# Kernel tuning notes

Hardware: AMD Instinct MI355X
Metric: run time of the kernel (lower is better)

The kernel has to match this reference:

```python
import jax, jax.numpy as jnp
import numpy as np

G = 512          # graphs per batch
NPG = 90         # nodes per graph (AAL-90 atlas)
N = G * NPG      # 46080 total nodes
DEG = 20
E = N * DEG      # 921600 edges
F_IN = 90
H = 64           # hidden_channels (args.hc)
K = 70           # sort-pool k


def setup_inputs() -> dict:
    key = jax.random.key(0)
    ks = jax.random.split(key, 14)
    x = jax.random.normal(ks[0], (N, F_IN), dtype=jnp.float32)
    # edges kept within each graph (realistic PyG batching)
    gid = jax.random.randint(ks[1], (E,), 0, G)
    src = gid * NPG + jax.random.randint(ks[2], (E,), 0, NPG)
    dst = gid * NPG + jax.random.randint(ks[3], (E,), 0, NPG)
    edge_index = jnp.stack([src, dst]).astype(jnp.int64)
    batch = (jnp.arange(N) // NPG).astype(jnp.int64)
    s_in = 1.0 / np.sqrt(F_IN)
    s_h = 1.0 / np.sqrt(H)
    s_p = 1.0 / np.sqrt(H * K)
    # SAGEConv: out = mean_aggr(x_j) @ W_l + x_i @ W_r + b
    W1l = jax.random.uniform(ks[4], (F_IN, H), jnp.float32, -s_in, s_in)
    W1r = jax.random.uniform(ks[5], (F_IN, H), jnp.float32, -s_in, s_in)
    b1 = jnp.zeros((H,), jnp.float32)
    W2l = jax.random.uniform(ks[6], (H, H), jnp.float32, -s_h, s_h)
    W2r = jax.random.uniform(ks[7], (H, H), jnp.float32, -s_h, s_h)
    b2 = jnp.zeros((H,), jnp.float32)
    Wl1 = jax.random.uniform(ks[8], (H * K, H), jnp.float32, -s_p, s_p)
    bl1 = jax.random.uniform(ks[9], (H,), jnp.float32, -s_p, s_p)
    Wl2 = jax.random.uniform(ks[10], (H, 1), jnp.float32, -s_h, s_h)
    bl2 = jax.random.uniform(ks[11], (1,), jnp.float32, -s_h, s_h)
    return {"x": x, "edge_index": edge_index, "batch": batch,
            "W1l": W1l, "W1r": W1r, "b1": b1,
            "W2l": W2l, "W2r": W2r, "b2": b2,
            "Wl1": Wl1, "bl1": bl1, "Wl2": Wl2, "bl2": bl2}


def sage_conv(x, src, dst, Wl, Wr, b):
    # gather source features, scatter-mean to destinations
    msg = x[src]                                              # [E, F]
    s = jax.ops.segment_sum(msg, dst, num_segments=N)         # [N, F]
    cnt = jax.ops.segment_sum(jnp.ones((src.shape[0], 1), x.dtype),
                              dst, num_segments=N)            # [N, 1]
    mean = s / jnp.maximum(cnt, 1.0)
    return mean @ Wl + x @ Wr + b


def global_sort_pool(x, k):
    # nodes per graph are contiguous and fixed (NPG >= k, no padding needed)
    xr = x.reshape(G, NPG, H)
    order = jnp.argsort(-xr[:, :, -1], axis=1)[:, :k]          # sort by last channel, desc
    top = jnp.take_along_axis(xr, order[:, :, None], axis=1)   # [G, k, H]
    return top.reshape(G, k * H)


def reference(x, edge_index, batch, W1l, W1r, b1, W2l, W2r, b2, Wl1, bl1, Wl2, bl2):
    src, dst = edge_index[0], edge_index[1]
    h = sage_conv(x, src, dst, W1l, W1r, b1)       # conv1
    x_train = h
    h = jax.nn.relu(h)
    h = sage_conv(h, src, dst, W2l, W2r, b2)       # conv2
    p = global_sort_pool(h, K)                     # [G, K*H]
    # dropout is identity at eval time
    p = p @ Wl1 + bl1
    p = p @ Wl2 + bl2
    out = jnp.squeeze(jax.nn.sigmoid(p))           # [G]
    return out, x_train
```

## Files before the change

### kernel.cpp

```cpp
#include <hip/hip_runtime.h>

typedef unsigned short u16;
typedef unsigned int u32;
typedef unsigned char u8;
typedef unsigned long long u64;

#define GG   512
#define NPG  90
#define NTOT (GG*NPG)
#define NED  921600
#define FIN  90
#define HC   64
#define KP   70
#define AW   23
#define AWG  (NPG*AW)

#define SAD  91
#define SP   68
#define SR   67

#define WF_W1L 0
#define WF_W1R 5760
#define WF_W2L 11520
#define WF_W2R 15616
#define WF_B1  19712
#define WF_B2  19776
#define WF_FOLD 19840
#define WF_ZC  24320
#define WF_FLAG 24321

__device__ __forceinline__ float bf2f(u16 u) {
    union { u32 i; float f; } v; v.i = ((u32)u) << 16; return v.f;
}
__device__ __forceinline__ float bflo(u32 u) {
    union { u32 i; float f; } v; v.i = u << 16; return v.f;
}
__device__ __forceinline__ float bfhi(u32 u) {
    union { u32 i; float f; } v; v.i = u & 0xFFFF0000u; return v.f;
}
__device__ __forceinline__ u16 f2bf(float f) {
    union { float f; u32 i; } v; v.f = f;
    u32 r = (v.i + 0x7FFFu + ((v.i >> 16) & 1u)) >> 16;
    return (u16)r;
}
__device__ __forceinline__ float ldadp(const void* p, long long i, int isf32) {
    return isf32 ? ((const float*)p)[i] : bf2f(((const u16*)p)[i]);
}

__global__ __launch_bounds__(256) void k_pre(
    const u32* __restrict__ xw, const int* __restrict__ ei,
    const void* W1l, const void* W1r, const void* b1,
    const void* W2l, const void* W2r, const void* b2,
    const void* Wl1, const void* bl1, const void* Wl2, const void* bl2,
    u32* __restrict__ A32, float* __restrict__ wf)
{
    __shared__ int sf;
    const int t = threadIdx.x;
    const int b = blockIdx.x;

    if (b < 900) {
        int lane = t & 63;
        u32 v = (lane < 16) ? (u32)ei[lane] : 0u;
        u64 bb = __ballot((lane & 1) && (v != 0));
        bool wide = (bb == 0ull);
        int e0 = b * 1024 + t * 4;
        int s[4], d[4];
        if (wide) {
            uint4 s01 = *(const uint4*)(ei + 2 * e0);
            uint4 s23 = *(const uint4*)(ei + 2 * e0 + 4);
            uint4 d01 = *(const uint4*)(ei + 2 * (NED + e0));
            uint4 d23 = *(const uint4*)(ei + 2 * (NED + e0) + 4);
            s[0] = (int)s01.x; s[1] = (int)s01.z; s[2] = (int)s23.x; s[3] = (int)s23.z;
            d[0] = (int)d01.x; d[1] = (int)d01.z; d[2] = (int)d23.x; d[3] = (int)d23.z;
        } else {
            uint4 ss = *(const uint4*)(ei + e0);
            uint4 dd = *(const uint4*)(ei + NED + e0);
            s[0] = (int)ss.x; s[1] = (int)ss.y; s[2] = (int)ss.z; s[3] = (int)ss.w;
            d[0] = (int)dd.x; d[1] = (int)dd.y; d[2] = (int)dd.z; d[3] = (int)dd.w;
        }
        #pragma unroll
        for (int k = 0; k < 4; ++k) {
            int dk = d[k];
            if ((unsigned)dk >= NTOT) continue;
            int g = (unsigned)dk / NPG;
            int dl = dk - g * NPG;
            int ls = s[k] - g * NPG;
            if ((unsigned)ls >= NPG) continue;
            atomicAdd(&A32[(size_t)g * AWG + dl * AW + (ls >> 2)],
                      1u << (8 * (ls & 3)));
        }
        return;
    }

    if (t < 64) {
        u32 e = (xw[t] >> 7) & 0xFF;
        u64 bb = __ballot(e >= 136);
        if (t == 0) sf = (bb != 0ull) ? 1 : 0;
    }
    __syncthreads();
    const int f32 = sf;

    if (b < 978) {
        int i = (b - 900) * 256 + t;
        if      (i < 5760)  wf[i] = ldadp(W1l, i, f32);
        else if (i < 11520) wf[i] = ldadp(W1r, i - 5760, f32);
        else if (i < 15616) wf[i] = ldadp(W2l, i - 11520, f32);
        else if (i < 19712) wf[i] = ldadp(W2r, i - 15616, f32);
        else if (i < 19776) wf[i] = ldadp(b1, i - 19712, f32);
        else if (i < 19840) wf[i] = ldadp(b2, i - 19776, f32);
        if (b == 900 && t == 0) wf[WF_FLAG] = f32 ? 1.0f : 0.0f;
    } else {
        int m = (b - 978) * 256 + t;
        if (m < 4480) {
            float s = 0.f;
            for (int j = 0; j < HC; ++j)
                s += ldadp(Wl1, (long long)m * HC + j, f32) * ldadp(Wl2, j, f32);
            wf[WF_FOLD + m] = s;
        } else if (m == 4480) {
            float s = ldadp(bl2, 0, f32);
            for (int j = 0; j < HC; ++j)
                s += ldadp(bl1, j, f32) * ldadp(Wl2, j, f32);
            wf[WF_ZC] = s;
        }
    }
}

__global__ __launch_bounds__(512, 4) void k_fused(
    const void* __restrict__ x, const u32* __restrict__ A32,
    const float* __restrict__ wf, void* __restrict__ dout)
{
    __shared__ __align__(16) char smem[58144];
    float* As    = (float*)smem;
    float* R1    = (float*)(smem + 32768);
    float* s_key = (float*)(smem + 57248);
    float* s_red = (float*)(smem + 57968);
    u16*   s_ord = (u16*)(smem + 58000);

    const int g = blockIdx.x;
    const int t = threadIdx.x;
    const bool isf32 = (wf[WF_FLAG] > 0.5f);

    const int l = t & 63;
    const int w = __builtin_amdgcn_readfirstlane(t >> 6);
    const int jb = w * 8;
    const int row0 = l;
    const bool has2 = (l < NPG - 64);
    const int row1 = has2 ? l + 64 : l;

    u32 abuf[5];
    {
        const u32* Ag = A32 + (size_t)g * AWG;
        #pragma unroll
        for (int j = 0; j < 5; ++j) {
            int p = t + j * 512;
            abuf[j] = (p < AWG) ? Ag[p] : 0u;
        }
    }

    if (isf32) {
        const float* xg = (const float*)x + (size_t)g * 8100;
        for (int p = t; p < 8100; p += 512) {
            int r = p / NPG, c = p - r * NPG;
            As[r * SAD + c] = xg[p];
        }
    } else {
        const u32* xg = (const u32*)((const u16*)x + (size_t)g * 8100);
        for (int p = t; p < 4050; p += 512) {
            int r = p / 45, c = (p - r * 45) * 2;
            u32 v = xg[p];
            As[r * SAD + c]     = bflo(v);
            As[r * SAD + c + 1] = bfhi(v);
        }
    }
    __syncthreads();

    float accP[2][8], accQ[2][8];
    {
        const float* bb = wf + WF_B1 + jb;
        #pragma unroll
        for (int j = 0; j < 8; ++j) {
            float bv = bb[j];
            accP[0][j] = 0.f; accP[1][j] = 0.f;
            accQ[0][j] = bv;  accQ[1][j] = bv;
        }
    }
    {
        const float* WL = wf + WF_W1L + jb;
        const float* WR = wf + WF_W1R + jb;
        #pragma unroll 3
        for (int k = 0; k < FIN; ++k) {
            float wl[8], wr[8];
            #pragma unroll
            for (int j = 0; j < 8; ++j) { wl[j] = WL[k * HC + j]; wr[j] = WR[k * HC + j]; }
            float x0 = As[row0 * SAD + k];
            float x1 = As[row1 * SAD + k];
            #pragma unroll
            for (int j = 0; j < 8; ++j) {
                accP[0][j] += x0 * wl[j]; accQ[0][j] += x0 * wr[j];
                accP[1][j] += x1 * wl[j]; accQ[1][j] += x1 * wr[j];
            }
        }
    }
    __syncthreads();

    *(float4*)(R1 + row0 * SP + jb)     = make_float4(accP[0][0], accP[0][1], accP[0][2], accP[0][3]);
    *(float4*)(R1 + row0 * SP + jb + 4) = make_float4(accP[0][4], accP[0][5], accP[0][6], accP[0][7]);
    if (has2) {
        *(float4*)(R1 + row1 * SP + jb)     = make_float4(accP[1][0], accP[1][1], accP[1][2], accP[1][3]);
        *(float4*)(R1 + row1 * SP + jb + 4) = make_float4(accP[1][4], accP[1][5], accP[1][6], accP[1][7]);
    }
    #pragma unroll
    for (int j = 0; j < 5; ++j) {
        int p = t + j * 512;
        if (p < AWG) {
            int r = p / AW, wc = p - r * AW;
            int c = wc * 4;
            u32 v = abuf[j];
            float* dst = As + r * SAD + c;
            dst[0] = (float)(v & 255u);
            dst[1] = (float)((v >> 8) & 255u);
            dst[2] = (float)((v >> 16) & 255u);
            if (c + 3 < SAD) dst[3] = (float)(v >> 24);
        }
    }
    __syncthreads();

    float r1v[2][8];
    float rc0, rc1;
    {
        float acc[2][8];
        float asum0 = 0.f, asum1 = 0.f;
        #pragma unroll
        for (int i = 0; i < 2; ++i)
            #pragma unroll
            for (int j = 0; j < 8; ++j) acc[i][j] = 0.f;
        for (int k = 0; k < NPG; ++k) {
            float4 p0 = *(const float4*)(R1 + k * SP + jb);
            float4 p1 = *(const float4*)(R1 + k * SP + jb + 4);
            float pv[8] = {p0.x,p0.y,p0.z,p0.w,p1.x,p1.y,p1.z,p1.w};
            float a0 = As[row0 * SAD + k];
            float a1 = As[row1 * SAD + k];
            asum0 += a0; asum1 += a1;
            #pragma unroll
            for (int j = 0; j < 8; ++j) {
                acc[0][j] += a0 * pv[j];
                acc[1][j] += a1 * pv[j];
            }
        }
        rc0 = 1.0f / fmaxf(asum0, 1.0f);
        rc1 = 1.0f / fmaxf(asum1, 1.0f);
        #pragma unroll
        for (int i = 0; i < 2; ++i) {
            if (i == 0 || has2) {
                int n = i ? row1 : row0;
                float rc = i ? rc1 : rc0;
                float h[8];
                #pragma unroll
                for (int j = 0; j < 8; ++j) h[j] = fmaf(rc, acc[i][j], accQ[i][j]);
                size_t base = 512 + (size_t)(g * NPG + n) * HC + jb;
                if (isf32) {
                    *(float4*)((float*)dout + base)     = make_float4(h[0],h[1],h[2],h[3]);
                    *(float4*)((float*)dout + base + 4) = make_float4(h[4],h[5],h[6],h[7]);
                } else {
                    uint4 pk;
                    pk.x = (u32)f2bf(h[0]) | ((u32)f2bf(h[1]) << 16);
                    pk.y = (u32)f2bf(h[2]) | ((u32)f2bf(h[3]) << 16);
                    pk.z = (u32)f2bf(h[4]) | ((u32)f2bf(h[5]) << 16);
                    pk.w = (u32)f2bf(h[6]) | ((u32)f2bf(h[7]) << 16);
                    *(uint4*)((u16*)dout + base) = pk;
                }
                #pragma unroll
                for (int j = 0; j < 8; ++j) r1v[i][j] = fmaxf(h[j], 0.f);
            }
        }
    }
    __syncthreads();
    #pragma unroll
    for (int j = 0; j < 8; ++j) R1[row0 * SR + jb + j] = r1v[0][j];
    if (has2) {
        #pragma unroll
        for (int j = 0; j < 8; ++j) R1[row1 * SR + jb + j] = r1v[1][j];
    }
    __syncthreads();

    {
        const float* bb = wf + WF_B2 + jb;
        #pragma unroll
        for (int j = 0; j < 8; ++j) {
            float bv = bb[j];
            accP[0][j] = 0.f; accP[1][j] = 0.f;
            accQ[0][j] = bv;  accQ[1][j] = bv;
        }
    }
    {
        const float* WL = wf + WF_W2L + jb;
        const float* WR = wf + WF_W2R + jb;
        #pragma unroll 4
        for (int k = 0; k < HC; ++k) {
            float wl[8], wr[8];
            #pragma unroll
            for (int j = 0; j < 8; ++j) { wl[j] = WL[k * HC + j]; wr[j] = WR[k * HC + j]; }
            float v0 = R1[row0 * SR + k];
            float v1 = R1[row1 * SR + k];
            #pragma unroll
            for (int j = 0; j < 8; ++j) {
                accP[0][j] += v0 * wl[j]; accQ[0][j] += v0 * wr[j];
                accP[1][j] += v1 * wl[j]; accQ[1][j] += v1 * wr[j];
            }
        }
    }
    __syncthreads();
    *(float4*)(R1 + row0 * SP + jb)     = make_float4(accP[0][0], accP[0][1], accP[0][2], accP[0][3]);
    *(float4*)(R1 + row0 * SP + jb + 4) = make_float4(accP[0][4], accP[0][5], accP[0][6], accP[0][7]);
    if (has2) {
        *(float4*)(R1 + row1 * SP + jb)     = make_float4(accP[1][0], accP[1][1], accP[1][2], accP[1][3]);
        *(float4*)(R1 + row1 * SP + jb + 4) = make_float4(accP[1][4], accP[1][5], accP[1][6], accP[1][7]);
    }
    __syncthreads();

    float h2v[2][8];
    {
        float acc[2][8];
        #pragma unroll
        for (int i = 0; i < 2; ++i)
            #pragma unroll
            for (int j = 0; j < 8; ++j) acc[i][j] = 0.f;
        for (int k = 0; k < NPG; ++k) {
            float4 p0 = *(const float4*)(R1 + k * SP + jb);
            float4 p1 = *(const float4*)(R1 + k * SP + jb + 4);
            float pv[8] = {p0.x,p0.y,p0.z,p0.w,p1.x,p1.y,p1.z,p1.w};
            float a0 = As[row0 * SAD + k];
            float a1 = As[row1 * SAD + k];
            #pragma unroll
            for (int j = 0; j < 8; ++j) {
                acc[0][j] += a0 * pv[j];
                acc[1][j] += a1 * pv[j];
            }
        }
        #pragma unroll
        for (int i = 0; i < 2; ++i) {
            if (i == 0 || has2) {
                int n = i ? row1 : row0;
                float rc = i ? rc1 : rc0;
                #pragma unroll
                for (int j = 0; j < 8; ++j)
                    h2v[i][j] = fmaf(rc, acc[i][j], accQ[i][j]);
                if (w == 7) s_key[n] = h2v[i][7];
            }
        }
    }
    __syncthreads();
    #pragma unroll
    for (int j = 0; j < 8; ++j) R1[row0 * SR + jb + j] = h2v[0][j];
    if (has2) {
        #pragma unroll
        for (int j = 0; j < 8; ++j) R1[row1 * SR + jb + j] = h2v[1][j];
    }
    if (t < NPG) {
        float my = s_key[t];
        int r = 0;
        for (int m2 = 0; m2 < NPG; ++m2) {
            float km = s_key[m2];
            r += (km > my) || (km == my && m2 < t);
        }
        if (r < KP) s_ord[r] = (u16)t;
    }
    __syncthreads();

    float zp = 0.f;
    for (int p = t; p < KP * HC; p += 512) {
        int i = p >> 6, c = p & 63;
        int nn = s_ord[i];
        zp += R1[nn * SR + c] * wf[WF_FOLD + p];
    }
    #pragma unroll
    for (int off = 32; off > 0; off >>= 1) zp += __shfl_down(zp, off);
    if ((t & 63) == 0) s_red[t >> 6] = zp;
    __syncthreads();
    if (t == 0) {
        float z = wf[WF_ZC];
        #pragma unroll
        for (int i = 0; i < 8; ++i) z += s_red[i];
        float sg = 1.0f / (1.0f + expf(-z));
        if (isf32) ((float*)dout)[g] = sg;
        else       ((u16*)dout)[g]   = f2bf(sg);
    }
}

extern "C" void kernel_launch(void* const* d_in, const int* in_sizes, int n_in,
                              void* d_out, int out_size, void* d_ws, size_t ws_size,
                              hipStream_t stream) {
    const void* x   = d_in[0];
    const int*  ei  = (const int*)d_in[1];
    const void* W1l = d_in[3];
    const void* W1r = d_in[4];
    const void* b1  = d_in[5];
    const void* W2l = d_in[6];
    const void* W2r = d_in[7];
    const void* b2  = d_in[8];
    const void* Wl1 = d_in[9];
    const void* bl1 = d_in[10];
    const void* Wl2 = d_in[11];
    const void* bl2 = d_in[12];

    char* ws    = (char*)d_ws;
    u32*  A32   = (u32*)ws;
    float* wf   = (float*)(ws + 4239360);

    hipMemsetAsync(A32, 0, 4239360, stream);
    k_pre<<<996, 256, 0, stream>>>((const u32*)x, ei, W1l, W1r, b1, W2l, W2r, b2,
                                   Wl1, bl1, Wl2, bl2, A32, wf);
    k_fused<<<GG, 512, 0, stream>>>(x, A32, wf, d_out);
}
```

Before: 183.1 us.

## Fuse memset, preprocessing and main kernel into one cooperative launch

Replaces the memset, the k_pre kernel and k_fused with a single cooperative kernel that uses grid.sync barriers. Each block zeroes its own adjacency slice, converts a share of the weights and loads its x tile, then after a grid sync scatters edges with atomics and, after a second sync, runs the shared compute pipeline. The aim is to remove launch gaps and the separate memset pass and to keep x resident in LDS. In exchange it relies on all 512 blocks being co-resident and adds two grid-wide barriers; the old three-launch path remains as a fallback if the cooperative launch fails.

```diff
diff --git a/kernel.cpp b/kernel.cpp
--- a/kernel.cpp
+++ b/kernel.cpp
@@ -1,4 +1,7 @@
 #include <hip/hip_runtime.h>
+#include <hip/hip_cooperative_groups.h>
+
+namespace cg = cooperative_groups;
 
 typedef unsigned short u16;
 typedef unsigned int u32;
@@ -45,6 +48,365 @@
 }
 __device__ __forceinline__ float ldadp(const void* p, long long i, int isf32) {
     return isf32 ? ((const float*)p)[i] : bf2f(((const u16*)p)[i]);
+}
+
+struct CParams {
+    const float* wf;
+    void* dout;
+    int g, t;
+    bool isf32;
+};
+
+__device__ __forceinline__ void pipeline_C(
+    float* As, float* R1, float* s_key, float* s_red, u16* s_ord,
+    const u32* abuf , const CParams& P)
+{
+    const int g = P.g, t = P.t;
+    const bool isf32 = P.isf32;
+    const float* wf = P.wf;
+    void* dout = P.dout;
+
+    const int l = t & 63;
+    const int w = __builtin_amdgcn_readfirstlane(t >> 6);
+    const int jb = w * 8;
+    const int row0 = l;
+    const bool has2 = (l < NPG - 64);
+    const int row1 = has2 ? l + 64 : l;
+
+    float accP[2][8], accQ[2][8];
+    {
+        const float* bb = wf + WF_B1 + jb;
+        #pragma unroll
+        for (int j = 0; j < 8; ++j) {
+            float bv = bb[j];
+            accP[0][j] = 0.f; accP[1][j] = 0.f;
+            accQ[0][j] = bv;  accQ[1][j] = bv;
+        }
+    }
+    {
+        const float* WL = wf + WF_W1L + jb;
+        const float* WR = wf + WF_W1R + jb;
+        #pragma unroll 3
+        for (int k = 0; k < FIN; ++k) {
+            float wl[8], wr[8];
+            #pragma unroll
+            for (int j = 0; j < 8; ++j) { wl[j] = WL[k * HC + j]; wr[j] = WR[k * HC + j]; }
+            float x0 = As[row0 * SAD + k];
+            float x1 = As[row1 * SAD + k];
+            #pragma unroll
+            for (int j = 0; j < 8; ++j) {
+                accP[0][j] += x0 * wl[j]; accQ[0][j] += x0 * wr[j];
+                accP[1][j] += x1 * wl[j]; accQ[1][j] += x1 * wr[j];
+            }
+        }
+    }
+    __syncthreads();
+
+    *(float4*)(R1 + row0 * SP + jb)     = make_float4(accP[0][0], accP[0][1], accP[0][2], accP[0][3]);
+    *(float4*)(R1 + row0 * SP + jb + 4) = make_float4(accP[0][4], accP[0][5], accP[0][6], accP[0][7]);
+    if (has2) {
+        *(float4*)(R1 + row1 * SP + jb)     = make_float4(accP[1][0], accP[1][1], accP[1][2], accP[1][3]);
+        *(float4*)(R1 + row1 * SP + jb + 4) = make_float4(accP[1][4], accP[1][5], accP[1][6], accP[1][7]);
+    }
+    #pragma unroll
+    for (int j = 0; j < 5; ++j) {
+        int p = t + j * 512;
+        if (p < AWG) {
+            int r = p / AW, wc = p - r * AW;
+            int c = wc * 4;
+            u32 v = abuf[j];
+            float* dst = As + r * SAD + c;
+            dst[0] = (float)(v & 255u);
+            dst[1] = (float)((v >> 8) & 255u);
+            dst[2] = (float)((v >> 16) & 255u);
+            if (c + 3 < SAD) dst[3] = (float)(v >> 24);
+        }
+    }
+    __syncthreads();
+
+    float r1v[2][8];
+    float rc0, rc1;
+    {
+        float acc[2][8];
+        float asum0 = 0.f, asum1 = 0.f;
+        #pragma unroll
+        for (int i = 0; i < 2; ++i)
+            #pragma unroll
+            for (int j = 0; j < 8; ++j) acc[i][j] = 0.f;
+        for (int k = 0; k < NPG; ++k) {
+            float4 p0 = *(const float4*)(R1 + k * SP + jb);
+            float4 p1 = *(const float4*)(R1 + k * SP + jb + 4);
+            float pv[8] = {p0.x,p0.y,p0.z,p0.w,p1.x,p1.y,p1.z,p1.w};
+            float a0 = As[row0 * SAD + k];
+            float a1 = As[row1 * SAD + k];
+            asum0 += a0; asum1 += a1;
+            #pragma unroll
+            for (int j = 0; j < 8; ++j) {
+                acc[0][j] += a0 * pv[j];
+                acc[1][j] += a1 * pv[j];
+            }
+        }
+        rc0 = 1.0f / fmaxf(asum0, 1.0f);
+        rc1 = 1.0f / fmaxf(asum1, 1.0f);
+        #pragma unroll
+        for (int i = 0; i < 2; ++i) {
+            if (i == 0 || has2) {
+                int n = i ? row1 : row0;
+                float rc = i ? rc1 : rc0;
+                float h[8];
+                #pragma unroll
+                for (int j = 0; j < 8; ++j) h[j] = fmaf(rc, acc[i][j], accQ[i][j]);
+                size_t base = 512 + (size_t)(g * NPG + n) * HC + jb;
+                if (isf32) {
+                    *(float4*)((float*)dout + base)     = make_float4(h[0],h[1],h[2],h[3]);
+                    *(float4*)((float*)dout + base + 4) = make_float4(h[4],h[5],h[6],h[7]);
+                } else {
+                    uint4 pk;
+                    pk.x = (u32)f2bf(h[0]) | ((u32)f2bf(h[1]) << 16);
+                    pk.y = (u32)f2bf(h[2]) | ((u32)f2bf(h[3]) << 16);
+                    pk.z = (u32)f2bf(h[4]) | ((u32)f2bf(h[5]) << 16);
+                    pk.w = (u32)f2bf(h[6]) | ((u32)f2bf(h[7]) << 16);
+                    *(uint4*)((u16*)dout + base) = pk;
+                }
+                #pragma unroll
+                for (int j = 0; j < 8; ++j) r1v[i][j] = fmaxf(h[j], 0.f);
+            }
+        }
+    }
+    __syncthreads();
+    #pragma unroll
+    for (int j = 0; j < 8; ++j) R1[row0 * SR + jb + j] = r1v[0][j];
+    if (has2) {
+        #pragma unroll
+        for (int j = 0; j < 8; ++j) R1[row1 * SR + jb + j] = r1v[1][j];
+    }
+    __syncthreads();
+
+    {
+        const float* bb = wf + WF_B2 + jb;
+        #pragma unroll
+        for (int j = 0; j < 8; ++j) {
+            float bv = bb[j];
+            accP[0][j] = 0.f; accP[1][j] = 0.f;
+            accQ[0][j] = bv;  accQ[1][j] = bv;
+        }
+    }
+    {
+        const float* WL = wf + WF_W2L + jb;
+        const float* WR = wf + WF_W2R + jb;
+        #pragma unroll 4
+        for (int k = 0; k < HC; ++k) {
+            float wl[8], wr[8];
+            #pragma unroll
+            for (int j = 0; j < 8; ++j) { wl[j] = WL[k * HC + j]; wr[j] = WR[k * HC + j]; }
+            float v0 = R1[row0 * SR + k];
+            float v1 = R1[row1 * SR + k];
+            #pragma unroll
+            for (int j = 0; j < 8; ++j) {
+                accP[0][j] += v0 * wl[j]; accQ[0][j] += v0 * wr[j];
+                accP[1][j] += v1 * wl[j]; accQ[1][j] += v1 * wr[j];
+            }
+        }
+    }
+    __syncthreads();
+    *(float4*)(R1 + row0 * SP + jb)     = make_float4(accP[0][0], accP[0][1], accP[0][2], accP[0][3]);
+    *(float4*)(R1 + row0 * SP + jb + 4) = make_float4(accP[0][4], accP[0][5], accP[0][6], accP[0][7]);
+    if (has2) {
+        *(float4*)(R1 + row1 * SP + jb)     = make_float4(accP[1][0], accP[1][1], accP[1][2], accP[1][3]);
+        *(float4*)(R1 + row1 * SP + jb + 4) = make_float4(accP[1][4], accP[1][5], accP[1][6], accP[1][7]);
+    }
+    __syncthreads();
+
+    float h2v[2][8];
+    {
+        float acc[2][8];
+        #pragma unroll
+        for (int i = 0; i < 2; ++i)
+            #pragma unroll
+            for (int j = 0; j < 8; ++j) acc[i][j] = 0.f;
+        for (int k = 0; k < NPG; ++k) {
+            float4 p0 = *(const float4*)(R1 + k * SP + jb);
+            float4 p1 = *(const float4*)(R1 + k * SP + jb + 4);
+            float pv[8] = {p0.x,p0.y,p0.z,p0.w,p1.x,p1.y,p1.z,p1.w};
+            float a0 = As[row0 * SAD + k];
+            float a1 = As[row1 * SAD + k];
+            #pragma unroll
+            for (int j = 0; j < 8; ++j) {
+                acc[0][j] += a0 * pv[j];
+                acc[1][j] += a1 * pv[j];
+            }
+        }
+        #pragma unroll
+        for (int i = 0; i < 2; ++i) {
+            if (i == 0 || has2) {
+                int n = i ? row1 : row0;
+                float rc = i ? rc1 : rc0;
+                #pragma unroll
+                for (int j = 0; j < 8; ++j)
+                    h2v[i][j] = fmaf(rc, acc[i][j], accQ[i][j]);
+                if (w == 7) s_key[n] = h2v[i][7];
+            }
+        }
+    }
+    __syncthreads();
+    #pragma unroll
+    for (int j = 0; j < 8; ++j) R1[row0 * SR + jb + j] = h2v[0][j];
+    if (has2) {
+        #pragma unroll
+        for (int j = 0; j < 8; ++j) R1[row1 * SR + jb + j] = h2v[1][j];
+    }
+    if (t < NPG) {
+        float my = s_key[t];
+        int r = 0;
+        for (int m2 = 0; m2 < NPG; ++m2) {
+            float km = s_key[m2];
+            r += (km > my) || (km == my && m2 < t);
+        }
+        if (r < KP) s_ord[r] = (u16)t;
+    }
+    __syncthreads();
+
+    float zp = 0.f;
+    for (int p = t; p < KP * HC; p += 512) {
+        int i = p >> 6, c = p & 63;
+        int nn = s_ord[i];
+        zp += R1[nn * SR + c] * wf[WF_FOLD + p];
+    }
+    #pragma unroll
+    for (int off = 32; off > 0; off >>= 1) zp += __shfl_down(zp, off);
+    if ((t & 63) == 0) s_red[t >> 6] = zp;
+    __syncthreads();
+    if (t == 0) {
+        float z = wf[WF_ZC];
+        #pragma unroll
+        for (int i = 0; i < 8; ++i) z += s_red[i];
+        float sg = 1.0f / (1.0f + expf(-z));
+        if (isf32) ((float*)dout)[g] = sg;
+        else       ((u16*)dout)[g]   = f2bf(sg);
+    }
+}
+
+__global__ __launch_bounds__(512, 4) void k_all(
+    const void* __restrict__ x, const int* __restrict__ ei,
+    const void* W1l, const void* W1r, const void* b1,
+    const void* W2l, const void* W2r, const void* b2,
+    const void* Wl1, const void* bl1, const void* Wl2, const void* bl2,
+    u32* __restrict__ A32, float* __restrict__ wf, void* __restrict__ dout)
+{
+    cg::grid_group grid = cg::this_grid();
+    __shared__ __align__(16) char smem[58144];
+    float* As    = (float*)smem;
+    float* R1    = (float*)(smem + 32768);
+    float* s_key = (float*)(smem + 57248);
+    int*   s_fl  = (int*)(smem + 57700);
+    float* s_red = (float*)(smem + 57968);
+    u16*   s_ord = (u16*)(smem + 58000);
+
+    const int g = blockIdx.x;
+    const int t = threadIdx.x;
+
+    if (t < 64) {
+        u32 e = (((const u32*)x)[t] >> 7) & 0xFF;
+        u64 bb = __ballot(e >= 136);
+        if (t == 0) s_fl[0] = (bb != 0ull) ? 1 : 0;
+    }
+    __syncthreads();
+    const bool isf32 = (s_fl[0] != 0);
+
+    {
+        u32* Ag = A32 + (size_t)g * AWG;
+        for (int p = t; p < AWG; p += 512) Ag[p] = 0u;
+    }
+    if (isf32) {
+        const float* xg = (const float*)x + (size_t)g * 8100;
+        for (int p = t; p < 8100; p += 512) {
+            int r = p / NPG, c = p - r * NPG;
+            As[r * SAD + c] = xg[p];
+        }
+    } else {
+        const u32* xg = (const u32*)((const u16*)x + (size_t)g * 8100);
+        for (int p = t; p < 4050; p += 512) {
+            int r = p / 45, c = (p - r * 45) * 2;
+            u32 v = xg[p];
+            As[r * SAD + c]     = bflo(v);
+            As[r * SAD + c + 1] = bfhi(v);
+        }
+    }
+    if (t < 39) {
+        int i = g * 39 + t;
+        if (i < 19840) {
+            float v;
+            if      (i < 5760)  v = ldadp(W1l, i, isf32);
+            else if (i < 11520) v = ldadp(W1r, i - 5760, isf32);
+            else if (i < 15616) v = ldadp(W2l, i - 11520, isf32);
+            else if (i < 19712) v = ldadp(W2r, i - 15616, isf32);
+            else if (i < 19776) v = ldadp(b1, i - 19712, isf32);
+            else                v = ldadp(b2, i - 19776, isf32);
+            wf[i] = v;
+        }
+    } else if (t >= 64 && t < 73) {
+        int m = g * 9 + (t - 64);
+        if (m < 4480) {
+            float s = 0.f;
+            for (int j = 0; j < HC; ++j)
+                s += ldadp(Wl1, (long long)m * HC + j, isf32) * ldadp(Wl2, j, isf32);
+            wf[WF_FOLD + m] = s;
+        } else if (m == 4480) {
+            float s = ldadp(bl2, 0, isf32);
+            for (int j = 0; j < HC; ++j)
+                s += ldadp(bl1, j, isf32) * ldadp(Wl2, j, isf32);
+            wf[WF_ZC] = s;
+        }
+    }
+    grid.sync();
+
+    {
+        int lane = t & 63;
+        u32 v = (lane < 16) ? (u32)ei[lane] : 0u;
+        u64 bb = __ballot((lane & 1) && (v != 0));
+        bool wide = (bb == 0ull);
+        if (t < 450) {
+            int e0 = g * 1800 + t * 4;
+            int s[4], d[4];
+            if (wide) {
+                uint4 s01 = *(const uint4*)(ei + 2 * e0);
+                uint4 s23 = *(const uint4*)(ei + 2 * e0 + 4);
+                uint4 d01 = *(const uint4*)(ei + 2 * (NED + e0));
+                uint4 d23 = *(const uint4*)(ei + 2 * (NED + e0) + 4);
+                s[0] = (int)s01.x; s[1] = (int)s01.z; s[2] = (int)s23.x; s[3] = (int)s23.z;
+                d[0] = (int)d01.x; d[1] = (int)d01.z; d[2] = (int)d23.x; d[3] = (int)d23.z;
+            } else {
+                uint4 ss = *(const uint4*)(ei + e0);
+                uint4 dd = *(const uint4*)(ei + NED + e0);
+                s[0] = (int)ss.x; s[1] = (int)ss.y; s[2] = (int)ss.z; s[3] = (int)ss.w;
+                d[0] = (int)dd.x; d[1] = (int)dd.y; d[2] = (int)dd.z; d[3] = (int)dd.w;
+            }
+            #pragma unroll
+            for (int k = 0; k < 4; ++k) {
+                int dk = d[k];
+                if ((unsigned)dk >= NTOT) continue;
+                int gg = (unsigned)dk / NPG;
+                int dl = dk - gg * NPG;
+                int ls = s[k] - gg * NPG;
+                if ((unsigned)ls >= NPG) continue;
+                atomicAdd(&A32[(size_t)gg * AWG + dl * AW + (ls >> 2)],
+                          1u << (8 * (ls & 3)));
+            }
+        }
+    }
+    grid.sync();
+
+    u32 abuf[5];
+    {
+        const u32* Ag = A32 + (size_t)g * AWG;
+        #pragma unroll
+        for (int j = 0; j < 5; ++j) {
+            int p = t + j * 512;
+            abuf[j] = (p < AWG) ? Ag[p] : 0u;
+        }
+    }
+    CParams P{wf, dout, g, t, isf32};
+    pipeline_C(As, R1, s_key, s_red, s_ord, abuf, P);
 }
 
 __global__ __launch_bounds__(256) void k_pre(
@@ -91,7 +453,6 @@
         }
         return;
     }
-
     if (t < 64) {
         u32 e = (xw[t] >> 7) & 0xFF;
         u64 bb = __ballot(e >= 136);
@@ -99,7 +460,6 @@
     }
     __syncthreads();
     const int f32 = sf;
-
     if (b < 978) {
         int i = (b - 900) * 256 + t;
         if      (i < 5760)  wf[i] = ldadp(W1l, i, f32);
@@ -140,13 +500,6 @@
     const int t = threadIdx.x;
     const bool isf32 = (wf[WF_FLAG] > 0.5f);
 
-    const int l = t & 63;
-    const int w = __builtin_amdgcn_readfirstlane(t >> 6);
-    const int jb = w * 8;
-    const int row0 = l;
-    const bool has2 = (l < NPG - 64);
-    const int row1 = has2 ? l + 64 : l;
-
     u32 abuf[5];
     {
         const u32* Ag = A32 + (size_t)g * AWG;
@@ -156,7 +509,6 @@
             abuf[j] = (p < AWG) ? Ag[p] : 0u;
         }
     }
-
     if (isf32) {
         const float* xg = (const float*)x + (size_t)g * 8100;
         for (int p = t; p < 8100; p += 512) {
@@ -173,218 +525,8 @@
         }
     }
     __syncthreads();
-
-    float accP[2][8], accQ[2][8];
-    {
-        const float* bb = wf + WF_B1 + jb;
-        #pragma unroll
-        for (int j = 0; j < 8; ++j) {
-            float bv = bb[j];
-            accP[0][j] = 0.f; accP[1][j] = 0.f;
-            accQ[0][j] = bv;  accQ[1][j] = bv;
-        }
-    }
-    {
-        const float* WL = wf + WF_W1L + jb;
-        const float* WR = wf + WF_W1R + jb;
-        #pragma unroll 3
-        for (int k = 0; k < FIN; ++k) {
-            float wl[8], wr[8];
-            #pragma unroll
-            for (int j = 0; j < 8; ++j) { wl[j] = WL[k * HC + j]; wr[j] = WR[k * HC + j]; }
-            float x0 = As[row0 * SAD + k];
-            float x1 = As[row1 * SAD + k];
-            #pragma unroll
-            for (int j = 0; j < 8; ++j) {
-                accP[0][j] += x0 * wl[j]; accQ[0][j] += x0 * wr[j];
-                accP[1][j] += x1 * wl[j]; accQ[1][j] += x1 * wr[j];
-            }
-        }
-    }
-    __syncthreads();
-
-    *(float4*)(R1 + row0 * SP + jb)     = make_float4(accP[0][0], accP[0][1], accP[0][2], accP[0][3]);
-    *(float4*)(R1 + row0 * SP + jb + 4) = make_float4(accP[0][4], accP[0][5], accP[0][6], accP[0][7]);
-    if (has2) {
-        *(float4*)(R1 + row1 * SP + jb)     = make_float4(accP[1][0], accP[1][1], accP[1][2], accP[1][3]);
-        *(float4*)(R1 + row1 * SP + jb + 4) = make_float4(accP[1][4], accP[1][5], accP[1][6], accP[1][7]);
-    }
-    #pragma unroll
-    for (int j = 0; j < 5; ++j) {
-        int p = t + j * 512;
-        if (p < AWG) {
-            int r = p / AW, wc = p - r * AW;
-            int c = wc * 4;
-            u32 v = abuf[j];
-            float* dst = As + r * SAD + c;
-            dst[0] = (float)(v & 255u);
-            dst[1] = (float)((v >> 8) & 255u);
-            dst[2] = (float)((v >> 16) & 255u);
-            if (c + 3 < SAD) dst[3] = (float)(v >> 24);
-        }
-    }
-    __syncthreads();
-
-    float r1v[2][8];
-    float rc0, rc1;
-    {
-        float acc[2][8];
-        float asum0 = 0.f, asum1 = 0.f;
-        #pragma unroll
-        for (int i = 0; i < 2; ++i)
-            #pragma unroll
-            for (int j = 0; j < 8; ++j) acc[i][j] = 0.f;
-        for (int k = 0; k < NPG; ++k) {
-            float4 p0 = *(const float4*)(R1 + k * SP + jb);
-            float4 p1 = *(const float4*)(R1 + k * SP + jb + 4);
-            float pv[8] = {p0.x,p0.y,p0.z,p0.w,p1.x,p1.y,p1.z,p1.w};
-            float a0 = As[row0 * SAD + k];
-            float a1 = As[row1 * SAD + k];
-            asum0 += a0; asum1 += a1;
-            #pragma unroll
-            for (int j = 0; j < 8; ++j) {
-                acc[0][j] += a0 * pv[j];
-                acc[1][j] += a1 * pv[j];
-            }
-        }
-        rc0 = 1.0f / fmaxf(asum0, 1.0f);
-        rc1 = 1.0f / fmaxf(asum1, 1.0f);
-        #pragma unroll
-        for (int i = 0; i < 2; ++i) {
-            if (i == 0 || has2) {
-                int n = i ? row1 : row0;
-                float rc = i ? rc1 : rc0;
-                float h[8];
-                #pragma unroll
-                for (int j = 0; j < 8; ++j) h[j] = fmaf(rc, acc[i][j], accQ[i][j]);
-                size_t base = 512 + (size_t)(g * NPG + n) * HC + jb;
-                if (isf32) {
-                    *(float4*)((float*)dout + base)     = make_float4(h[0],h[1],h[2],h[3]);
-                    *(float4*)((float*)dout + base + 4) = make_float4(h[4],h[5],h[6],h[7]);
-                } else {
-                    uint4 pk;
-                    pk.x = (u32)f2bf(h[0]) | ((u32)f2bf(h[1]) << 16);
-                    pk.y = (u32)f2bf(h[2]) | ((u32)f2bf(h[3]) << 16);
-                    pk.z = (u32)f2bf(h[4]) | ((u32)f2bf(h[5]) << 16);
-                    pk.w = (u32)f2bf(h[6]) | ((u32)f2bf(h[7]) << 16);
-                    *(uint4*)((u16*)dout + base) = pk;
-                }
-                #pragma unroll
-                for (int j = 0; j < 8; ++j) r1v[i][j] = fmaxf(h[j], 0.f);
-            }
-        }
-    }
-    __syncthreads();
-    #pragma unroll
-    for (int j = 0; j < 8; ++j) R1[row0 * SR + jb + j] = r1v[0][j];
-    if (has2) {
-        #pragma unroll
-        for (int j = 0; j < 8; ++j) R1[row1 * SR + jb + j] = r1v[1][j];
-    }
-    __syncthreads();
-
-    {
-        const float* bb = wf + WF_B2 + jb;
-        #pragma unroll
-        for (int j = 0; j < 8; ++j) {
-            float bv = bb[j];
-            accP[0][j] = 0.f; accP[1][j] = 0.f;
-            accQ[0][j] = bv;  accQ[1][j] = bv;
-        }
-    }
-    {
-        const float* WL = wf + WF_W2L + jb;
-        const float* WR = wf + WF_W2R + jb;
-        #pragma unroll 4
-        for (int k = 0; k < HC; ++k) {
-            float wl[8], wr[8];
-            #pragma unroll
-            for (int j = 0; j < 8; ++j) { wl[j] = WL[k * HC + j]; wr[j] = WR[k * HC + j]; }
-            float v0 = R1[row0 * SR + k];
-            float v1 = R1[row1 * SR + k];
-            #pragma unroll
-            for (int j = 0; j < 8; ++j) {
-                accP[0][j] += v0 * wl[j]; accQ[0][j] += v0 * wr[j];
-                accP[1][j] += v1 * wl[j]; accQ[1][j] += v1 * wr[j];
-            }
-        }
-    }
-    __syncthreads();
-    *(float4*)(R1 + row0 * SP + jb)     = make_float4(accP[0][0], accP[0][1], accP[0][2], accP[0][3]);
-    *(float4*)(R1 + row0 * SP + jb + 4) = make_float4(accP[0][4], accP[0][5], accP[0][6], accP[0][7]);
-    if (has2) {
-        *(float4*)(R1 + row1 * SP + jb)     = make_float4(accP[1][0], accP[1][1], accP[1][2], accP[1][3]);
-        *(float4*)(R1 + row1 * SP + jb + 4) = make_float4(accP[1][4], accP[1][5], accP[1][6], accP[1][7]);
-    }
-    __syncthreads();
-
-    float h2v[2][8];
-    {
-        float acc[2][8];
-        #pragma unroll
-        for (int i = 0; i < 2; ++i)
-            #pragma unroll
-            for (int j = 0; j < 8; ++j) acc[i][j] = 0.f;
-        for (int k = 0; k < NPG; ++k) {
-            float4 p0 = *(const float4*)(R1 + k * SP + jb);
-            float4 p1 = *(const float4*)(R1 + k * SP + jb + 4);
-            float pv[8] = {p0.x,p0.y,p0.z,p0.w,p1.x,p1.y,p1.z,p1.w};
-            float a0 = As[row0 * SAD + k];
-            float a1 = As[row1 * SAD + k];
-            #pragma unroll
-            for (int j = 0; j < 8; ++j) {
-                acc[0][j] += a0 * pv[j];
-                acc[1][j] += a1 * pv[j];
-            }
-        }
-        #pragma unroll
-        for (int i = 0; i < 2; ++i) {
-            if (i == 0 || has2) {
-                int n = i ? row1 : row0;
-                float rc = i ? rc1 : rc0;
-                #pragma unroll
-                for (int j = 0; j < 8; ++j)
-                    h2v[i][j] = fmaf(rc, acc[i][j], accQ[i][j]);
-                if (w == 7) s_key[n] = h2v[i][7];
-            }
-        }
-    }
-    __syncthreads();
-    #pragma unroll
-    for (int j = 0; j < 8; ++j) R1[row0 * SR + jb + j] = h2v[0][j];
-    if (has2) {
-        #pragma unroll
-        for (int j = 0; j < 8; ++j) R1[row1 * SR + jb + j] = h2v[1][j];
-    }
-    if (t < NPG) {
-        float my = s_key[t];
-        int r = 0;
-        for (int m2 = 0; m2 < NPG; ++m2) {
-            float km = s_key[m2];
-            r += (km > my) || (km == my && m2 < t);
-        }
-        if (r < KP) s_ord[r] = (u16)t;
-    }
-    __syncthreads();
-
-    float zp = 0.f;
-    for (int p = t; p < KP * HC; p += 512) {
-        int i = p >> 6, c = p & 63;
-        int nn = s_ord[i];
-        zp += R1[nn * SR + c] * wf[WF_FOLD + p];
-    }
-    #pragma unroll
-    for (int off = 32; off > 0; off >>= 1) zp += __shfl_down(zp, off);
-    if ((t & 63) == 0) s_red[t >> 6] = zp;
-    __syncthreads();
-    if (t == 0) {
-        float z = wf[WF_ZC];
-        #pragma unroll
-        for (int i = 0; i < 8; ++i) z += s_red[i];
-        float sg = 1.0f / (1.0f + expf(-z));
-        if (isf32) ((float*)dout)[g] = sg;
-        else       ((u16*)dout)[g]   = f2bf(sg);
-    }
+    CParams P{wf, dout, g, t, isf32};
+    pipeline_C(As, R1, s_key, s_red, s_ord, abuf, P);
 }
 
 extern "C" void kernel_launch(void* const* d_in, const int* in_sizes, int n_in,
@@ -403,12 +545,20 @@
     const void* Wl2 = d_in[11];
     const void* bl2 = d_in[12];
 
-    char* ws    = (char*)d_ws;
-    u32*  A32   = (u32*)ws;
-    float* wf   = (float*)(ws + 4239360);
-
-    hipMemsetAsync(A32, 0, 4239360, stream);
-    k_pre<<<996, 256, 0, stream>>>((const u32*)x, ei, W1l, W1r, b1, W2l, W2r, b2,
-                                   Wl1, bl1, Wl2, bl2, A32, wf);
-    k_fused<<<GG, 512, 0, stream>>>(x, A32, wf, d_out);
-}
+    char* ws   = (char*)d_ws;
+    u32*  A32  = (u32*)ws;
+    float* wf  = (float*)(ws + 4239360);
+    void* out  = d_out;
+
+    void* args[] = { (void*)&x, (void*)&ei, (void*)&W1l, (void*)&W1r, (void*)&b1,
+                     (void*)&W2l, (void*)&W2r, (void*)&b2, (void*)&Wl1, (void*)&bl1,
+                     (void*)&Wl2, (void*)&bl2, (void*)&A32, (void*)&wf, (void*)&out };
+    hipError_t err = hipLaunchCooperativeKernel((void*)k_all, dim3(GG), dim3(512),
+                                                args, 0, stream);
+    if (err != hipSuccess) {
+        hipMemsetAsync(A32, 0, 4239360, stream);
+        k_pre<<<996, 256, 0, stream>>>((const u32*)x, ei, W1l, W1r, b1, W2l, W2r, b2,
+                                       Wl1, bl1, Wl2, bl2, A32, wf);
+        k_fused<<<GG, 512, 0, stream>>>(x, A32, wf, d_out);
+    }
+}
```

Result: slower. 339.8 us (+85.6%).
